# Optimization experiments

Hardware: AMD Instinct MI355X
Metric: run time of the kernel (lower is better)

Reference implementation:

```python
import jax, jax.numpy as jnp
from jax import lax
import numpy as np

OUT_CH = 16      # texture_features
INTER = 32       # texture_features_intermediate
TEXDIM = 1024    # texture_dimensions
IN_SIZE = 76


def _leaky(x):
    return jnp.where(x >= 0, x, 0.02 * x)


def grid_sample_bilinear_border(tex, grid):
    """torch.nn.functional.grid_sample, mode='bilinear', padding_mode='border',
    align_corners=False.  tex: (N,C,H,W); grid: (N,Ho,Wo,2) with (x,y) in [-1,1].
    N == 1 here; vectorized over H,W via fancy indexing."""
    N, C, H, W = tex.shape
    x, y = grid[..., 0], grid[..., 1]
    # unnormalize (align_corners=False)
    ix = ((x + 1.0) * W - 1.0) * 0.5
    iy = ((y + 1.0) * H - 1.0) * 0.5
    # border padding: clamp continuous coords
    ix = jnp.clip(ix, 0.0, W - 1.0)
    iy = jnp.clip(iy, 0.0, H - 1.0)
    x0 = jnp.floor(ix); y0 = jnp.floor(iy)
    wx = ix - x0; wy = iy - y0
    x0i = jnp.clip(x0, 0, W - 1).astype(jnp.int32)
    x1i = jnp.clip(x0 + 1, 0, W - 1).astype(jnp.int32)
    y0i = jnp.clip(y0, 0, H - 1).astype(jnp.int32)
    y1i = jnp.clip(y0 + 1, 0, H - 1).astype(jnp.int32)
    t = tex[0]  # (C,H,W)
    v00 = t[:, y0i[0], x0i[0]]  # (C,Ho,Wo)
    v01 = t[:, y0i[0], x1i[0]]
    v10 = t[:, y1i[0], x0i[0]]
    v11 = t[:, y1i[0], x1i[0]]
    wx = wx[0][None]; wy = wy[0][None]  # (1,Ho,Wo) broadcast over C
    out = (v00 * (1 - wx) * (1 - wy) + v01 * wx * (1 - wy)
           + v10 * (1 - wx) * wy + v11 * wx * wy)
    return out[None]  # (1,C,Ho,Wo)


def setup_inputs() -> dict:
    key = jax.random.key(0)
    ks = jax.random.split(key, 11)
    expressions = jax.random.normal(ks[0], (1, IN_SIZE), jnp.float32)
    audio_features = jax.random.normal(ks[1], (1, 16), jnp.float32)
    uv_inputs = jax.random.uniform(ks[2], (1, 2, 1024, 1024), jnp.float32, -1.0, 1.0)
    data = jax.random.normal(ks[3], (1, INTER, TEXDIM, TEXDIM), jnp.float32)
    def lin(kw, kb, fo, fi):
        s = 1.0 / np.sqrt(fi).astype(np.float32)
        return (jax.random.uniform(kw, (fo, fi), jnp.float32, -s, s),
                jax.random.uniform(kb, (fo,), jnp.float32, -s, s))
    W1, b1 = lin(ks[4], ks[5], 128, IN_SIZE)
    W2, b2 = lin(ks[6], ks[7], 64, 128)
    W3, b3 = lin(ks[8], ks[9], OUT_CH * 4 * 4 * INTER, 64)
    return {"expressions": expressions, "audio_features": audio_features,
            "uv_inputs": uv_inputs, "data": data,
            "W1": W1, "b1": b1, "W2": W2, "b2": b2, "W3": W3, "b3": b3}


def reference(expressions, audio_features, uv_inputs, data, W1, b1, W2, b2, W3, b3):
    # tiny MLP -> dynamic 4x4 conv filter
    h = expressions.reshape(1, 1, -1)
    h = _leaky(h @ W1.T + b1)
    h = _leaky(h @ W2.T + b2)
    f = jnp.tanh(h @ W3.T + b3)
    conv_filter = f.reshape(OUT_CH, INTER, 4, 4)
    # conv2d(data, filter, stride=1, padding=2) -> (1, OUT_CH, D+1, D+1)
    tex_eval = lax.conv_general_dilated(
        data, conv_filter, window_strides=(1, 1), padding=((2, 2), (2, 2)),
        dimension_numbers=("NCHW", "OIHW", "NCHW"))
    # grid: stack x (chan 0) and y (chan 1) along last dim
    grid = jnp.stack([uv_inputs[:, 0], uv_inputs[:, 1]], axis=3)  # (1,Ho,Wo,2)
    return grid_sample_bilinear_border(tex_eval, grid)
```

## Files before the change

### kernel.cpp

```cpp
#include <hip/hip_runtime.h>
#include <math.h>

#define NPX   1048576
#define TD    1025
#define PW    35
#define PH    19
#define DPAD  1028
#define ROWB  65792
#define DP_OFF 33673216

typedef _Float16 half8 __attribute__((ext_vector_type(8)));
typedef float    f32x4 __attribute__((ext_vector_type(4)));

__device__ __forceinline__ void load_lds16(const void* g, void* lds) {
    __builtin_amdgcn_global_load_lds(
        (const __attribute__((address_space(1))) void*)g,
        (__attribute__((address_space(3))) void*)lds, 16, 0, 0);
}

__global__ __launch_bounds__(256) void mlp_kernel(
    const float* __restrict__ expr,
    const float* __restrict__ W1, const float* __restrict__ b1,
    const float* __restrict__ W2, const float* __restrict__ b2,
    const float* __restrict__ W3, const float* __restrict__ b3,
    _Float16* __restrict__ ffrag_g)
{
    __shared__ float sx[76];
    __shared__ float sh1[128];
    __shared__ float sh2[64];
    int t = threadIdx.x;
    if (t < 76) sx[t] = expr[t];
    __syncthreads();
    if (t < 128) {
        float a = b1[t];
        const float* w = W1 + t * 76;
        #pragma unroll 4
        for (int i = 0; i < 76; ++i) a += sx[i] * w[i];
        sh1[t] = a >= 0.f ? a : 0.02f * a;
    }
    __syncthreads();
    if (t < 64) {
        float a = b2[t];
        const float* w = W2 + t * 128;
        #pragma unroll 4
        for (int i = 0; i < 128; ++i) a += sh1[i] * w[i];
        sh2[t] = a >= 0.f ? a : 0.02f * a;
    }
    __syncthreads();
    int o = blockIdx.x * 256 + t;
    float a = b3[o];
    const float* w = W3 + o * 64;
    #pragma unroll 4
    for (int i = 0; i < 64; ++i) a += sh2[i] * w[i];
    a = tanhf(a);
    int oc = o >> 9;
    int ic = (o >> 4) & 31;
    int kk = o & 15;
    ffrag_g[(size_t)(kk * 64 + (ic >> 3) * 16 + oc) * 8 + (ic & 7)] = (_Float16)a;
}

__global__ __launch_bounds__(256) void repack_kernel(
    const float* __restrict__ data, _Float16* __restrict__ Dp)
{
    __shared__ _Float16 s[256 * 32];
    int tid = threadIdx.x;
    int Y = blockIdx.y;
    int X = blockIdx.x * 256 + tid;
    int y = Y - 2, x = X - 2;
    bool ok = ((unsigned)y < 1024u) && ((unsigned)x < 1024u);
    const float* dp = data + ((size_t)y << 10) + x;

    float v[32];
    #pragma unroll
    for (int j = 0; j < 32; ++j) v[j] = 0.f;
    if (ok) {
        #pragma unroll
        for (int j = 0; j < 32; ++j) v[j] = __builtin_nontemporal_load(&dp[(size_t)j * NPX]);
    }
    #pragma unroll
    for (int g = 0; g < 4; ++g) {
        half8 h;
        #pragma unroll
        for (int j = 0; j < 8; ++j) h[j] = (_Float16)v[g * 8 + j];
        int chunk = tid * 4 + g;
        int sw = chunk ^ ((chunk >> 3) & 7);
        *(half8*)((char*)s + sw * 16) = h;
    }
    __syncthreads();
    char* rowbase = (char*)Dp + (size_t)Y * ROWB + blockIdx.x * 16384;
    int lim = ROWB - blockIdx.x * 16384;
    #pragma unroll
    for (int i = 0; i < 4; ++i) {
        int off = tid * 16 + i * 4096;
        if (off < lim) {
            int chunk = tid + i * 256;
            int sw = chunk ^ ((chunk >> 3) & 7);
            *(uint4*)(rowbase + off) = *(uint4*)((char*)s + sw * 16);
        }
    }
}

__global__ __launch_bounds__(256, 3) void conv_mfma_kernel(
    const _Float16* __restrict__ Dp,
    const _Float16* __restrict__ ffrag_g,
    _Float16* __restrict__ tex)
{
    __shared__ _Float16 sp[PH * PW * 32];

    int tid = threadIdx.x;
    int l = tid & 63, w = tid >> 6;
    int ox0 = blockIdx.x * 32;
    int oy0 = blockIdx.y * 16;

    half8 bfrag[16];
    #pragma unroll
    for (int kk = 0; kk < 16; ++kk)
        bfrag[kk] = *(const half8*)&ffrag_g[kk * 512 + l * 8];

    for (int r = w; r < PH; r += 4) {
        int gy = min(oy0 + r, DPAD - 1);
        const char* grow = (const char*)Dp + (size_t)gy * ROWB;
        _Float16* lrow = sp + r * (PW * 32);
        #pragma unroll
        for (int c = 0; c < 3; ++c) {
            int off = ox0 * 64 + c * 1024 + l * 16;
            off = min(off, ROWB - 16);
            if (c < 2 || l < 12)
                load_lds16(grow + off, (char*)lrow + c * 1024);
        }
    }
    __syncthreads();

    int lane15 = l & 15;
    int q = l >> 4;

    f32x4 acc[8];
    #pragma unroll
    for (int t = 0; t < 8; ++t) acc[t] = (f32x4){0.f, 0.f, 0.f, 0.f};

    #pragma unroll 4
    for (int kk = 0; kk < 16; ++kk) {
        int ky = kk >> 2, kx = kk & 3;
        #pragma unroll
        for (int t = 0; t < 8; ++t) {
            int pc = (w * 4 + (t >> 1) + ky) * PW + (t & 1) * 16 + lane15 + kx;
            half8 af = *(half8*)&sp[pc * 32 + q * 8];
            acc[t] = __builtin_amdgcn_mfma_f32_16x16x32_f16(af, bfrag[kk], acc[t], 0, 0, 0);
        }
    }

    #pragma unroll
    for (int t = 0; t < 8; ++t) {
        int oy = oy0 + w * 4 + (t >> 1);
        if (oy > 1024) continue;
        int pxb = ox0 + (t & 1) * 16 + q * 4;
        #pragma unroll
        for (int r = 0; r < 4; ++r) {
            int px = pxb + r;
            if (px > 1024) continue;
            tex[((size_t)oy * TD + px) * 16 + lane15] = (_Float16)acc[t][r];
        }
    }
}

__global__ __launch_bounds__(256, 6) void sample_kernel(
    const float* __restrict__ uv,
    const _Float16* __restrict__ tex,
    float* __restrict__ out)
{
    int p = blockIdx.x * 256 + threadIdx.x;
    float x = __builtin_nontemporal_load(&uv[p]);
    float y = __builtin_nontemporal_load(&uv[NPX + p]);
    float ix = fminf(fmaxf(((x + 1.f) * 1025.f - 1.f) * 0.5f, 0.f), 1024.f);
    float iy = fminf(fmaxf(((y + 1.f) * 1025.f - 1.f) * 0.5f, 0.f), 1024.f);
    float fx0 = floorf(ix), fy0 = floorf(iy);
    float wx = ix - fx0, wy = iy - fy0;
    int x0 = (int)fx0, y0 = (int)fy0;
    int x1 = min(x0 + 1, 1024), y1 = min(y0 + 1, 1024);

    const half8* t00 = (const half8*)(tex + ((size_t)y0 * TD + x0) * 16);
    const half8* t01 = (const half8*)(tex + ((size_t)y0 * TD + x1) * 16);
    const half8* t10 = (const half8*)(tex + ((size_t)y1 * TD + x0) * 16);
    const half8* t11 = (const half8*)(tex + ((size_t)y1 * TD + x1) * 16);

    half8 v0 = t00[0], v1 = t00[1];
    half8 v2 = t01[0], v3 = t01[1];
    half8 v4 = t10[0], v5 = t10[1];
    half8 v6 = t11[0], v7 = t11[1];

    float w00 = (1.f - wx) * (1.f - wy);
    float w01 = wx * (1.f - wy);
    float w10 = (1.f - wx) * wy;
    float w11 = wx * wy;

    #pragma unroll
    for (int c = 0; c < 8; ++c) {
        float r0 = (float)v0[c] * w00 + (float)v2[c] * w01
                 + (float)v4[c] * w10 + (float)v6[c] * w11;
        float r1 = (float)v1[c] * w00 + (float)v3[c] * w01
                 + (float)v5[c] * w10 + (float)v7[c] * w11;
        __builtin_nontemporal_store(r0, &out[(size_t)c * NPX + p]);
        __builtin_nontemporal_store(r1, &out[(size_t)(c + 8) * NPX + p]);
    }
}

extern "C" void kernel_launch(void* const* d_in, const int* in_sizes, int n_in,
                              void* d_out, int out_size, void* d_ws, size_t ws_size,
                              hipStream_t stream) {
    const float* expr = (const float*)d_in[0];
    const float* uv   = (const float*)d_in[2];
    const float* data = (const float*)d_in[3];
    const float* W1   = (const float*)d_in[4];
    const float* b1   = (const float*)d_in[5];
    const float* W2   = (const float*)d_in[6];
    const float* b2   = (const float*)d_in[7];
    const float* W3   = (const float*)d_in[8];
    const float* b3   = (const float*)d_in[9];
    float* out = (float*)d_out;

    _Float16* ffrag_g  = (_Float16*)d_ws;
    _Float16* tex      = (_Float16*)((char*)d_ws + 49152);
    _Float16* Dp       = (_Float16*)((char*)d_ws + DP_OFF);

    mlp_kernel<<<32, 256, 0, stream>>>(expr, W1, b1, W2, b2, W3, b3, ffrag_g);
    repack_kernel<<<dim3(5, DPAD), 256, 0, stream>>>(data, Dp);
    conv_mfma_kernel<<<dim3(33, 65), 256, 0, stream>>>(Dp, ffrag_g, tex);
    sample_kernel<<<NPX / 256, 256, 0, stream>>>(uv, tex, out);
}
```

Baseline: 362.4 us.

## Fuse MLP into repack kernel and split conv staging into two overlapped halves

The MLP blocks are appended to the repack grid so one launch does both, which removes a kernel launch and the serialization between the two. The conv kernel now stages its input tile as two 16-column strips in separate LDS buffers. It issues the right strip's async global-to-LDS load before computing on the left strip, so part of the load latency overlaps with MFMA work. In exchange the kernel uses slightly more LDS and adds a second barrier, and the strips re-read overlapping halo columns.

```diff
diff --git a/kernel.cpp b/kernel.cpp
--- a/kernel.cpp
+++ b/kernel.cpp
@@ -3,8 +3,9 @@
 
 #define NPX   1048576
 #define TD    1025
-#define PW    35
 #define PH    19
+#define SCELL 19
+#define SROW  (SCELL * 32)
 #define DPAD  1028
 #define ROWB  65792
 #define DP_OFF 33673216
@@ -18,54 +19,57 @@
         (__attribute__((address_space(3))) void*)lds, 16, 0, 0);
 }
 
-__global__ __launch_bounds__(256) void mlp_kernel(
+__global__ __launch_bounds__(256) void repack_mlp_kernel(
+    const float* __restrict__ data, _Float16* __restrict__ Dp,
     const float* __restrict__ expr,
     const float* __restrict__ W1, const float* __restrict__ b1,
     const float* __restrict__ W2, const float* __restrict__ b2,
     const float* __restrict__ W3, const float* __restrict__ b3,
     _Float16* __restrict__ ffrag_g)
 {
-    __shared__ float sx[76];
-    __shared__ float sh1[128];
-    __shared__ float sh2[64];
-    int t = threadIdx.x;
-    if (t < 76) sx[t] = expr[t];
-    __syncthreads();
-    if (t < 128) {
-        float a = b1[t];
-        const float* w = W1 + t * 76;
+    __shared__ char smem[16384];
+    int tid = threadIdx.x;
+    int b = blockIdx.x;
+
+    if (b >= 5140) {
+        float* sx  = (float*)smem;
+        float* sh1 = sx + 80;
+        float* sh2 = sh1 + 128;
+        if (tid < 76) sx[tid] = expr[tid];
+        __syncthreads();
+        if (tid < 128) {
+            float a = b1[tid];
+            const float* w = W1 + tid * 76;
+            #pragma unroll 4
+            for (int i = 0; i < 76; ++i) a += sx[i] * w[i];
+            sh1[tid] = a >= 0.f ? a : 0.02f * a;
+        }
+        __syncthreads();
+        if (tid < 64) {
+            float a = b2[tid];
+            const float* w = W2 + tid * 128;
+            #pragma unroll 4
+            for (int i = 0; i < 128; ++i) a += sh1[i] * w[i];
+            sh2[tid] = a >= 0.f ? a : 0.02f * a;
+        }
+        __syncthreads();
+        int o = (b - 5140) * 256 + tid;
+        float a = b3[o];
+        const float* w = W3 + o * 64;
         #pragma unroll 4
-        for (int i = 0; i < 76; ++i) a += sx[i] * w[i];
-        sh1[t] = a >= 0.f ? a : 0.02f * a;
-    }
-    __syncthreads();
-    if (t < 64) {
-        float a = b2[t];
-        const float* w = W2 + t * 128;
-        #pragma unroll 4
-        for (int i = 0; i < 128; ++i) a += sh1[i] * w[i];
-        sh2[t] = a >= 0.f ? a : 0.02f * a;
-    }
-    __syncthreads();
-    int o = blockIdx.x * 256 + t;
-    float a = b3[o];
-    const float* w = W3 + o * 64;
-    #pragma unroll 4
-    for (int i = 0; i < 64; ++i) a += sh2[i] * w[i];
-    a = tanhf(a);
-    int oc = o >> 9;
-    int ic = (o >> 4) & 31;
-    int kk = o & 15;
-    ffrag_g[(size_t)(kk * 64 + (ic >> 3) * 16 + oc) * 8 + (ic & 7)] = (_Float16)a;
-}
-
-__global__ __launch_bounds__(256) void repack_kernel(
-    const float* __restrict__ data, _Float16* __restrict__ Dp)
-{
-    __shared__ _Float16 s[256 * 32];
-    int tid = threadIdx.x;
-    int Y = blockIdx.y;
-    int X = blockIdx.x * 256 + tid;
+        for (int i = 0; i < 64; ++i) a += sh2[i] * w[i];
+        a = tanhf(a);
+        int oc = o >> 9;
+        int ic = (o >> 4) & 31;
+        int kk = o & 15;
+        ffrag_g[(size_t)(kk * 64 + (ic >> 3) * 16 + oc) * 8 + (ic & 7)] = (_Float16)a;
+        return;
+    }
+
+    _Float16* s = (_Float16*)smem;
+    int xb = b % 5;
+    int Y  = b / 5;
+    int X = xb * 256 + tid;
     int y = Y - 2, x = X - 2;
     bool ok = ((unsigned)y < 1024u) && ((unsigned)x < 1024u);
     const float* dp = data + ((size_t)y << 10) + x;
@@ -87,8 +91,8 @@
         *(half8*)((char*)s + sw * 16) = h;
     }
     __syncthreads();
-    char* rowbase = (char*)Dp + (size_t)Y * ROWB + blockIdx.x * 16384;
-    int lim = ROWB - blockIdx.x * 16384;
+    char* rowbase = (char*)Dp + (size_t)Y * ROWB + xb * 16384;
+    int lim = ROWB - xb * 16384;
     #pragma unroll
     for (int i = 0; i < 4; ++i) {
         int off = tid * 16 + i * 4096;
@@ -100,65 +104,86 @@
     }
 }
 
+__device__ __forceinline__ void stage_strip(
+    const _Float16* __restrict__ Dp, _Float16* sp,
+    int ox0, int oy0, int w, int l, int xoff)
+{
+    int base = (ox0 + xoff) * 64;
+    for (int r = w; r < PH; r += 4) {
+        int gy = min(oy0 + r, DPAD - 1);
+        const char* grow = (const char*)Dp + (size_t)gy * ROWB;
+        char* lrow = (char*)(sp + r * SROW);
+        int off0 = min(base + l * 16, ROWB - 16);
+        load_lds16(grow + off0, lrow);
+        if (l < 12) {
+            int off1 = min(base + 1024 + l * 16, ROWB - 16);
+            load_lds16(grow + off1, lrow + 1024);
+        }
+    }
+}
+
+__device__ __forceinline__ void compute_strip(
+    const _Float16* sp, const half8* bfrag, f32x4* acc,
+    int w, int lane15, int q)
+{
+    #pragma unroll 4
+    for (int kk = 0; kk < 16; ++kk) {
+        int ky = kk >> 2, kx = kk & 3;
+        #pragma unroll
+        for (int tr = 0; tr < 4; ++tr) {
+            int pc = (w * 4 + tr + ky) * SCELL + lane15 + kx;
+            half8 af = *(const half8*)&sp[pc * 32 + q * 8];
+            acc[tr] = __builtin_amdgcn_mfma_f32_16x16x32_f16(af, bfrag[kk], acc[tr], 0, 0, 0);
+        }
+    }
+}
+
 __global__ __launch_bounds__(256, 3) void conv_mfma_kernel(
     const _Float16* __restrict__ Dp,
     const _Float16* __restrict__ ffrag_g,
     _Float16* __restrict__ tex)
 {
-    __shared__ _Float16 sp[PH * PW * 32];
+    __shared__ _Float16 spL[PH * SROW];
+    __shared__ _Float16 spR[PH * SROW];
 
     int tid = threadIdx.x;
     int l = tid & 63, w = tid >> 6;
     int ox0 = blockIdx.x * 32;
     int oy0 = blockIdx.y * 16;
+    int lane15 = l & 15;
+    int q = l >> 4;
 
     half8 bfrag[16];
     #pragma unroll
     for (int kk = 0; kk < 16; ++kk)
         bfrag[kk] = *(const half8*)&ffrag_g[kk * 512 + l * 8];
 
-    for (int r = w; r < PH; r += 4) {
-        int gy = min(oy0 + r, DPAD - 1);
-        const char* grow = (const char*)Dp + (size_t)gy * ROWB;
-        _Float16* lrow = sp + r * (PW * 32);
-        #pragma unroll
-        for (int c = 0; c < 3; ++c) {
-            int off = ox0 * 64 + c * 1024 + l * 16;
-            off = min(off, ROWB - 16);
-            if (c < 2 || l < 12)
-                load_lds16(grow + off, (char*)lrow + c * 1024);
-        }
-    }
+    f32x4 acc[2][4];
+    #pragma unroll
+    for (int p = 0; p < 2; ++p)
+        #pragma unroll
+        for (int t = 0; t < 4; ++t) acc[p][t] = (f32x4){0.f, 0.f, 0.f, 0.f};
+
+    stage_strip(Dp, spL, ox0, oy0, w, l, 0);
     __syncthreads();
-
-    int lane15 = l & 15;
-    int q = l >> 4;
-
-    f32x4 acc[8];
-    #pragma unroll
-    for (int t = 0; t < 8; ++t) acc[t] = (f32x4){0.f, 0.f, 0.f, 0.f};
-
-    #pragma unroll 4
-    for (int kk = 0; kk < 16; ++kk) {
-        int ky = kk >> 2, kx = kk & 3;
-        #pragma unroll
-        for (int t = 0; t < 8; ++t) {
-            int pc = (w * 4 + (t >> 1) + ky) * PW + (t & 1) * 16 + lane15 + kx;
-            half8 af = *(half8*)&sp[pc * 32 + q * 8];
-            acc[t] = __builtin_amdgcn_mfma_f32_16x16x32_f16(af, bfrag[kk], acc[t], 0, 0, 0);
-        }
-    }
-
-    #pragma unroll
-    for (int t = 0; t < 8; ++t) {
-        int oy = oy0 + w * 4 + (t >> 1);
-        if (oy > 1024) continue;
-        int pxb = ox0 + (t & 1) * 16 + q * 4;
-        #pragma unroll
-        for (int r = 0; r < 4; ++r) {
-            int px = pxb + r;
-            if (px > 1024) continue;
-            tex[((size_t)oy * TD + px) * 16 + lane15] = (_Float16)acc[t][r];
+    stage_strip(Dp, spR, ox0, oy0, w, l, 16);
+    compute_strip(spL, bfrag, acc[0], w, lane15, q);
+    __syncthreads();
+    compute_strip(spR, bfrag, acc[1], w, lane15, q);
+
+    #pragma unroll
+    for (int p = 0; p < 2; ++p) {
+        #pragma unroll
+        for (int tr = 0; tr < 4; ++tr) {
+            int oy = oy0 + w * 4 + tr;
+            if (oy > 1024) continue;
+            int pxb = ox0 + p * 16 + q * 4;
+            #pragma unroll
+            for (int r = 0; r < 4; ++r) {
+                int px = pxb + r;
+                if (px > 1024) continue;
+                tex[((size_t)oy * TD + px) * 16 + lane15] = (_Float16)acc[p][tr][r];
+            }
         }
     }
 }
@@ -222,8 +247,8 @@
     _Float16* tex      = (_Float16*)((char*)d_ws + 49152);
     _Float16* Dp       = (_Float16*)((char*)d_ws + DP_OFF);
 
-    mlp_kernel<<<32, 256, 0, stream>>>(expr, W1, b1, W2, b2, W3, b3, ffrag_g);
-    repack_kernel<<<dim3(5, DPAD), 256, 0, stream>>>(data, Dp);
+    repack_mlp_kernel<<<5140 + 32, 256, 0, stream>>>(
+        data, Dp, expr, W1, b1, W2, b2, W3, b3, ffrag_g);
     conv_mfma_kernel<<<dim3(33, 65), 256, 0, stream>>>(Dp, ffrag_g, tex);
     sample_kernel<<<NPX / 256, 256, 0, stream>>>(uv, tex, out);
 }
```

After: 374.2 us. 3.2% more time.
